# Kernel tuning notes

Hardware: AMD Instinct MI355X
Metric: run time of the kernel (lower is better)

The kernel has to match this reference:

```python
import jax, jax.numpy as jnp
import numpy as np

IN, H, OUT, T, B = 132, 1024, 132, 100, 256


def setup_inputs() -> dict:
    key = jax.random.key(0)
    ks = jax.random.split(key, 16)
    s_in = 1.0 / np.sqrt(H)
    def mk(k, shape):
        return jax.random.uniform(k, shape, jnp.float32, -s_in, s_in)
    inp = {
        "real_seq": jax.random.normal(ks[0], (B, T, IN), jnp.float32),
        "W_ih1": mk(ks[1], (4 * H, IN)), "W_hh1": mk(ks[2], (4 * H, H)),
        "b_ih1": mk(ks[3], (4 * H,)),   "b_hh1": mk(ks[4], (4 * H,)),
        "W_ih2": mk(ks[5], (4 * H, H)), "W_hh2": mk(ks[6], (4 * H, H)),
        "b_ih2": mk(ks[7], (4 * H,)),   "b_hh2": mk(ks[8], (4 * H,)),
        "W_ih3": mk(ks[9], (4 * H, H)), "W_hh3": mk(ks[10], (4 * H, H)),
        "b_ih3": mk(ks[11], (4 * H,)),  "b_hh3": mk(ks[12], (4 * H,)),
        "W_dec": mk(ks[13], (OUT, H)),  "b_dec": mk(ks[14], (OUT,)),
        "condition_num": 5, "groundtruth_num": 5,
    }
    return inp


def _lstm_cell(x, h, c, W_ih, W_hh, b_ih, b_hh):
    # torch LSTMCell: gates in (i, f, g, o) order
    gates = x @ W_ih.T + b_ih + h @ W_hh.T + b_hh
    i, f, g, o = jnp.split(gates, 4, axis=-1)
    i, f, o = jax.nn.sigmoid(i), jax.nn.sigmoid(f), jax.nn.sigmoid(o)
    g = jnp.tanh(g)
    c_new = f * c + i * g
    h_new = o * jnp.tanh(c_new)
    return h_new, c_new


def reference(real_seq, W_ih1, W_hh1, b_ih1, b_hh1,
              W_ih2, W_hh2, b_ih2, b_hh2,
              W_ih3, W_hh3, b_ih3, b_hh3,
              W_dec, b_dec, condition_num, groundtruth_num):
    batch, seq_len, _ = real_seq.shape
    # static teacher-forcing schedule: [1]*gt_num + [0]*cond_num, tiled
    gt = np.ones((100, groundtruth_num)); con = np.zeros((100, condition_num))
    cond = jnp.asarray(np.concatenate((gt, con), 1).reshape(-1)[:seq_len] == 1)

    z = jnp.zeros((batch, H), jnp.float32)
    init = (z, z, z, z, z, z, jnp.zeros((batch, OUT), jnp.float32))

    def step(carry, xs):
        h0, h1, h2, c0, c1, c2, prev_out = carry
        frame, use_gt = xs
        x = jnp.where(use_gt, frame, prev_out)
        # note: lstm2/lstm3 consume the OLD h0/h1, faithful to forward_lstm
        nh0, nc0 = _lstm_cell(x,  h0, c0, W_ih1, W_hh1, b_ih1, b_hh1)
        nh1, nc1 = _lstm_cell(h0, h1, c1, W_ih2, W_hh2, b_ih2, b_hh2)
        nh2, nc2 = _lstm_cell(h1, h2, c2, W_ih3, W_hh3, b_ih3, b_hh3)
        out = nh2 @ W_dec.T + b_dec
        return (nh0, nh1, nh2, nc0, nc1, nc2, out), out

    xs = (jnp.swapaxes(real_seq, 0, 1), cond)  # [T,B,IN], [T]
    _, outs = jax.lax.scan(step, init, xs)      # outs: [T,B,OUT]
    # torch concatenates along dim 1 each step -> [B, T*OUT]
    return jnp.swapaxes(outs, 0, 1).reshape(batch, seq_len * OUT)
```

## Files before the change

### kernel.cpp

```cpp
#include <hip/hip_runtime.h>
#include <math.h>

#define B_   256
#define T_   100
#define IN_  132
#define OUT_ 132
#define H_   1024
#define BH   ((size_t)B_ * H_)
#define WSZ  ((size_t)4096 * H_)

typedef _Float16 f16;
typedef _Float16 f16x8 __attribute__((ext_vector_type(8)));
typedef float    f32x4 __attribute__((ext_vector_type(4)));

#define MFMA16(a, b, c) __builtin_amdgcn_mfma_f32_16x16x32_f16((a), (b), (c), 0, 0, 0)

#define AS1 __attribute__((address_space(1)))
#define AS3 __attribute__((address_space(3)))

__device__ __forceinline__ void gl_lds16(const void* g, void* l) {
    __builtin_amdgcn_global_load_lds((AS1 void*)g, (AS3 void*)l, 16, 0, 0);
}

__device__ __forceinline__ float sigmoidf_(float x) {
    return 1.0f / (1.0f + __expf(-x));
}
__device__ __forceinline__ float tanhf_(float x) {
    float e = __expf(2.0f * x);
    return 1.0f - 2.0f / (e + 1.0f);
}


__global__ void conv_pad(const float* __restrict__ src, f16* __restrict__ dst,
                         int src_rows, int src_k, int dst_k) {
    int k = blockIdx.x * 256 + threadIdx.x;
    int r = blockIdx.y;
    if (k >= dst_k) return;
    float v = (r < src_rows && k < src_k) ? src[(size_t)r * src_k + k] : 0.0f;
    dst[(size_t)r * dst_k + k] = (f16)v;
}

__global__ void seq_pad(const float* __restrict__ src, f16* __restrict__ dst) {
    int k  = threadIdx.x;
    int bt = blockIdx.y;
    if (k >= 160) return;
    float v = (k < IN_) ? src[(size_t)bt * IN_ + k] : 0.0f;
    dst[(size_t)bt * 160 + k] = (f16)v;
}

__global__ void convT_kernel(const float* __restrict__ Wd, f16* __restrict__ WdT) {
    int k = blockIdx.x * 256 + threadIdx.x;
    int m = blockIdx.y;
    if (k >= 160) return;
    float v = (k < IN_) ? Wd[(size_t)k * H_ + m] : 0.0f;
    WdT[(size_t)m * 160 + k] = (f16)v;
}

__global__ void bias_add_kernel(const float* __restrict__ a, const float* __restrict__ b,
                                float* __restrict__ dst, int n) {
    int i = blockIdx.x * 256 + threadIdx.x;
    if (i < n) dst[i] = a[i] + b[i];
}

__global__ void bfb_kernel(const float* __restrict__ Wih1, const float* __restrict__ bd,
                           float* __restrict__ bfb) {
    int j = blockIdx.x * 256 + threadIdx.x;
    if (j >= 4096) return;
    float s = 0.0f;
    for (int k = 0; k < IN_; ++k) s += Wih1[(size_t)j * IN_ + k] * bd[k];
    bfb[j] = s;
}

__global__ void zero_kernel(float* __restrict__ p, int n) {
    int i = blockIdx.x * blockDim.x + threadIdx.x;
    int st = gridDim.x * blockDim.x;
    for (; i < n; i += st) p[i] = 0.0f;
}

__global__ __launch_bounds__(256) void wfb_mfma(
    const f16* __restrict__ W0, const f16* __restrict__ WdT, f16* __restrict__ Wfb)
{
    const int m0 = blockIdx.x * 128;
    const int n0 = blockIdx.y * 128;
    const int tid  = threadIdx.x;
    const int lane = tid & 63;
    const int w    = tid >> 6;
    const int lx   = lane & 15;
    const int quad = lane >> 4;
    const int wrow = w >> 1, wcol = w & 1;

    __shared__ __align__(16) char lds[32768];

    auto stA = [&](int kt, int buf) {
        char* base = lds + buf * 16384;
#pragma unroll
        for (int i = 0; i < 2; ++i) {
            int r  = w * 32 + i * 16 + (lane >> 2);
            int sg = (lane & 3) ^ (r & 3);
            const f16* g = W0 + (size_t)(m0 + r) * 160 + kt * 32 + sg * 8;
            gl_lds16(g, base + (size_t)(w * 32 + i * 16) * 64);
        }
    };
    auto stB = [&](int kt, int buf) {
        char* base = lds + 8192 + buf * 16384;
#pragma unroll
        for (int i = 0; i < 2; ++i) {
            int r  = w * 32 + i * 16 + (lane >> 2);
            int sg = (lane & 3) ^ (r & 3);
            const f16* g = WdT + (size_t)(n0 + r) * 160 + kt * 32 + sg * 8;
            gl_lds16(g, base + (size_t)(w * 32 + i * 16) * 64);
        }
    };

    f32x4 acc[4][4];
#pragma unroll
    for (int m = 0; m < 4; ++m)
#pragma unroll
        for (int n = 0; n < 4; ++n) acc[m][n] = (f32x4){0.f, 0.f, 0.f, 0.f};

    stA(0, 0); stB(0, 0);
    for (int kt = 0; kt < 5; ++kt) {
        __syncthreads();
        if (kt + 1 < 5) { stA(kt + 1, (kt + 1) & 1); stB(kt + 1, (kt + 1) & 1); }
        const char* bA = lds + (kt & 1) * 16384;
        const char* bB = lds + 8192 + (kt & 1) * 16384;
        f16x8 af[4], bf[4];
#pragma unroll
        for (int m = 0; m < 4; ++m) {
            int R = wrow * 64 + m * 16 + lx;
            af[m] = *(const f16x8*)(bA + R * 64 + ((quad ^ (R & 3)) * 16));
        }
#pragma unroll
        for (int n = 0; n < 4; ++n) {
            int R = wcol * 64 + n * 16 + lx;
            bf[n] = *(const f16x8*)(bB + R * 64 + ((quad ^ (R & 3)) * 16));
        }
#pragma unroll
        for (int m = 0; m < 4; ++m)
#pragma unroll
            for (int n = 0; n < 4; ++n)
                acc[m][n] = MFMA16(af[m], bf[n], acc[m][n]);
    }

#pragma unroll
    for (int m = 0; m < 4; ++m)
#pragma unroll
        for (int n = 0; n < 4; ++n)
#pragma unroll
            for (int r = 0; r < 4; ++r) {
                int row = m0 + wrow * 64 + m * 16 + quad * 4 + r;
                int col = n0 + wcol * 64 + n * 16 + lx;
                Wfb[(size_t)row * H_ + col] = (f16)acc[m][n][r];
            }
}

__global__ __launch_bounds__(256) void step_mfma(
    const f16* __restrict__ seq16,
    const f16* __restrict__ hfb,
    const f16* __restrict__ h2old,
    const f16* __restrict__ h01c,
    f16* __restrict__ h01n,
    f16* __restrict__ h2out,
    float* __restrict__ c_st,
    const f16* __restrict__ W0,
    const f16* __restrict__ Wb,
    const f16* __restrict__ Wfb,
    const float* __restrict__ bias_comb,
    const float* __restrict__ bfb,
    const int* __restrict__ cnum, const int* __restrict__ gnum,
    int t)
{
    const int j0   = blockIdx.x * 32;
    const int mb   = blockIdx.y;
    const int l    = blockIdx.z;
    const int tid  = threadIdx.x;
    const int lane = tid & 63;
    const int w    = tid >> 6;
    const int lx   = lane & 15;
    const int quad = lane >> 4;
    const int wrow = w >> 1, wcol = w & 1;

    __shared__ __align__(16) char lds[49152];

    bool use_gt = false;
    int n0 = 32;
    size_t ldA0 = H_, ldB0 = H_;
    const f16 *Ap0 = nullptr, *Wp0 = nullptr;
    if (l == 0) {
        int cn = cnum[0], gn = gnum[0];
        use_gt = (t % (cn + gn)) < gn;
        if (use_gt)      { Ap0 = seq16 + (size_t)t * 160; ldA0 = (size_t)T_ * 160;
                           Wp0 = W0; ldB0 = 160; n0 = 5; }
        else if (t == 0) { n0 = 0; }
        else             { Ap0 = hfb; Wp0 = Wfb; }
    } else if (l == 1) { Ap0 = h01c;      Wp0 = Wb + 1 * WSZ; }
    else               { Ap0 = h01c + BH; Wp0 = Wb + 3 * WSZ; }
    const f16* Ap1 = (l == 0) ? h01c : (l == 1) ? (h01c + BH) : h2old;
    const f16* Wp1 = Wb + (size_t)((l == 0) ? 0 : (l == 1) ? 2 : 4) * WSZ;
    const int ntot = n0 + 32;

    auto stA = [&](const f16* Ap, size_t ldA, int kk, int buf) {
        char* base = lds + buf * 12288 + w * 1024;
        int row = w * 16 + (lane >> 2);
        int sg  = (lane & 3) ^ (row & 3);
        const f16* g = Ap + (size_t)(mb * 64 + row) * ldA + kk * 32 + sg * 8;
        gl_lds16(g, base);
    };
    auto stB = [&](const f16* Wp, size_t ldk, int kk, int buf) {
        char* base = lds + buf * 12288 + 4096;
#pragma unroll
        for (int i = 0; i < 2; ++i) {
            int c    = w * 32 + i * 16 + (lane >> 2);
            int sg   = (lane & 3) ^ (c & 3);
            int gate = (c >> 4) & 3;
            int jj   = (c & 15) + (c >> 6) * 16;
            const f16* g = Wp + (size_t)(gate * H_ + j0 + jj) * ldk + kk * 32 + sg * 8;
            gl_lds16(g, base + (size_t)(w * 32 + i * 16) * 64);
        }
    };
    auto stage = [&](int kt, int buf) {
        if (kt < n0) {
            stA(Ap0, ldA0, kt, buf);
            stB(Wp0, ldB0, kt, buf);
        } else {
            stA(Ap1, (size_t)H_, kt - n0, buf);
            stB(Wp1, (size_t)H_, kt - n0, buf);
        }
    };

    f32x4 acc[2][4];
#pragma unroll
    for (int m = 0; m < 2; ++m)
#pragma unroll
        for (int n = 0; n < 4; ++n) acc[m][n] = (f32x4){0.f, 0.f, 0.f, 0.f};

    stage(0, 0);
    stage(1, 1);
    stage(2, 2);

    for (int kt = 0; kt < ntot; ++kt) {
        if (kt < ntot - 2)       asm volatile("s_waitcnt vmcnt(6)" ::: "memory");
        else if (kt == ntot - 2) asm volatile("s_waitcnt vmcnt(3)" ::: "memory");
        else                     asm volatile("s_waitcnt vmcnt(0)" ::: "memory");
        __builtin_amdgcn_s_barrier();

        const char* bA = lds + (kt & 3) * 12288;
        const char* bB = bA + 4096;
        f16x8 af[2], bf[4];
#pragma unroll
        for (int m = 0; m < 2; ++m) {
            int R = wrow * 32 + m * 16 + lx;
            af[m] = *(const f16x8*)(bA + R * 64 + ((quad ^ (R & 3)) * 16));
        }
#pragma unroll
        for (int n = 0; n < 4; ++n) {
            int R = wcol * 64 + n * 16 + lx;
            bf[n] = *(const f16x8*)(bB + R * 64 + ((quad ^ (R & 3)) * 16));
        }
        asm volatile("s_waitcnt lgkmcnt(0)" ::: "memory");
        __builtin_amdgcn_sched_barrier(0);
        __builtin_amdgcn_s_barrier();

        if (kt + 3 < ntot) stage(kt + 3, (kt + 3) & 3);

        __builtin_amdgcn_s_setprio(1);
#pragma unroll
        for (int m = 0; m < 2; ++m)
#pragma unroll
            for (int n = 0; n < 4; ++n)
                acc[m][n] = MFMA16(af[m], bf[n], acc[m][n]);
        __builtin_amdgcn_s_setprio(0);
    }

    const int j = j0 + wcol * 16 + lx;
    const float* bc = bias_comb + l * 4096;
    const bool addfb = (l == 0 && !use_gt && t > 0);
    float bi  = bc[j]        + (addfb ? bfb[j]        : 0.f);
    float bff = bc[1024 + j] + (addfb ? bfb[1024 + j] : 0.f);
    float bg  = bc[2048 + j] + (addfb ? bfb[2048 + j] : 0.f);
    float bo  = bc[3072 + j] + (addfb ? bfb[3072 + j] : 0.f);
#pragma unroll
    for (int m = 0; m < 2; ++m) {
#pragma unroll
        for (int r = 0; r < 4; ++r) {
            int b = mb * 64 + wrow * 32 + m * 16 + quad * 4 + r;
            float gi = acc[m][0][r] + bi;
            float gf = acc[m][1][r] + bff;
            float gg = acc[m][2][r] + bg;
            float go = acc[m][3][r] + bo;
            size_t ix = ((size_t)l * B_ + b) * H_ + j;
            float cn = sigmoidf_(gf) * c_st[ix] + sigmoidf_(gi) * tanhf_(gg);
            c_st[ix] = cn;
            float hv = sigmoidf_(go) * tanhf_(cn);
            if (l == 2) h2out[(size_t)b * H_ + j] = (f16)hv;
            else        h01n[(size_t)l * BH + (size_t)b * H_ + j] = (f16)hv;
        }
    }
}

__global__ __launch_bounds__(256) void decode_mfma(
    const f16* __restrict__ hist,
    const f16* __restrict__ Wd16,
    const float* __restrict__ bd,
    float* __restrict__ dout)
{
    const int r0  = blockIdx.x * 128;
    const int nb0 = blockIdx.y * 32;
    const int tid  = threadIdx.x;
    const int lane = tid & 63;
    const int w    = tid >> 6;
    const int lx   = lane & 15;
    const int quad = lane >> 4;

    __shared__ __align__(16) char lds[20480];

    auto stA = [&](int kt, int buf) {
        char* base = lds + buf * 10240;
#pragma unroll
        for (int i = 0; i < 2; ++i) {
            int r  = w * 32 + i * 16 + (lane >> 2);
            int sg = (lane & 3) ^ (r & 3);
            const f16* g = hist + (size_t)(r0 + r) * H_ + kt * 32 + sg * 8;
            gl_lds16(g, base + (size_t)(w * 32 + i * 16) * 64);
        }
    };
    auto stB = [&](int kt, int buf) {
        char* base = lds + 8192 + buf * 10240;
        if (w < 2) {
            int r  = w * 16 + (lane >> 2);
            int sg = (lane & 3) ^ (r & 3);
            const f16* g = Wd16 + (size_t)(nb0 + r) * H_ + kt * 32 + sg * 8;
            gl_lds16(g, base + (size_t)(w * 16) * 64);
        }
    };

    f32x4 acc[2][2];
#pragma unroll
    for (int m = 0; m < 2; ++m)
#pragma unroll
        for (int n = 0; n < 2; ++n) acc[m][n] = (f32x4){0.f, 0.f, 0.f, 0.f};

    stA(0, 0); stB(0, 0);
    for (int kt = 0; kt < 32; ++kt) {
        __syncthreads();
        if (kt + 1 < 32) { stA(kt + 1, (kt + 1) & 1); stB(kt + 1, (kt + 1) & 1); }
        const char* bA = lds + (kt & 1) * 10240;
        const char* bB = lds + 8192 + (kt & 1) * 10240;
        f16x8 af[2], bf[2];
#pragma unroll
        for (int m = 0; m < 2; ++m) {
            int R = w * 32 + m * 16 + lx;
            af[m] = *(const f16x8*)(bA + R * 64 + ((quad ^ (R & 3)) * 16));
        }
#pragma unroll
        for (int n = 0; n < 2; ++n) {
            int R = n * 16 + lx;
            bf[n] = *(const f16x8*)(bB + R * 64 + ((quad ^ (R & 3)) * 16));
        }
#pragma unroll
        for (int m = 0; m < 2; ++m)
#pragma unroll
            for (int n = 0; n < 2; ++n)
                acc[m][n] = MFMA16(af[m], bf[n], acc[m][n]);
    }

#pragma unroll
    for (int n = 0; n < 2; ++n) {
        int nn = nb0 + n * 16 + lx;
        if (nn < OUT_) {
            float bv = bd[nn];
#pragma unroll
            for (int m = 0; m < 2; ++m)
#pragma unroll
                for (int r = 0; r < 4; ++r) {
                    int row = r0 + w * 32 + m * 16 + quad * 4 + r;
                    int tt = row >> 8, b = row & 255;
                    dout[(size_t)b * (T_ * OUT_) + (size_t)tt * OUT_ + nn] = acc[m][n][r] + bv;
                }
        }
    }
}


extern "C" void kernel_launch(void* const* d_in, const int* in_sizes, int n_in,
                              void* d_out, int out_size, void* d_ws, size_t ws_size,
                              hipStream_t stream) {
    const float* seq  = (const float*)d_in[0];
    const float* Wih1 = (const float*)d_in[1];
    const float* Whh1 = (const float*)d_in[2];
    const float* bih1 = (const float*)d_in[3];
    const float* bhh1 = (const float*)d_in[4];
    const float* Wih2 = (const float*)d_in[5];
    const float* Whh2 = (const float*)d_in[6];
    const float* bih2 = (const float*)d_in[7];
    const float* bhh2 = (const float*)d_in[8];
    const float* Wih3 = (const float*)d_in[9];
    const float* Whh3 = (const float*)d_in[10];
    const float* bih3 = (const float*)d_in[11];
    const float* bhh3 = (const float*)d_in[12];
    const float* Wd   = (const float*)d_in[13];
    const float* bd   = (const float*)d_in[14];
    const int*   cnum = (const int*)d_in[15];
    const int*   gnum = (const int*)d_in[16];

    char* p = (char*)d_ws;
    f16*  W0   = (f16*)p;  p += (size_t)4096 * 160 * 2;
    f16*  Wb   = (f16*)p;  p += (size_t)5 * 4096 * 1024 * 2;
    f16*  Wd16 = (f16*)p;  p += (size_t)160 * 1024 * 2;
    f16*  WdT  = (f16*)p;  p += (size_t)1024 * 160 * 2;
    f16*  Wfb  = (f16*)p;  p += (size_t)4096 * 1024 * 2;
    float* bias_comb = (float*)p; p += (size_t)3 * 4096 * 4;
    float* bfb = (float*)p; p += (size_t)4096 * 4;
    f16*  hist = (f16*)p;  p += (size_t)100 * BH * 2;
    f16*  h01a = (f16*)p;  p += (size_t)2 * BH * 2;
    f16*  h01b = (f16*)p;  p += (size_t)2 * BH * 2;
    float* c_st = (float*)p; p += (size_t)3 * BH * 4;
    f16*  seq16 = (f16*)p; p += (size_t)B_ * T_ * 160 * 2;
    const int zero_floats = (int)(((size_t)4 * BH * 2 + (size_t)3 * BH * 4) / 4);

    conv_pad<<<dim3(1, 4096), 256, 0, stream>>>(Wih1, W0, 4096, IN_, 160);
    conv_pad<<<dim3(4, 4096), 256, 0, stream>>>(Whh1, Wb + 0 * WSZ, 4096, H_, H_);
    conv_pad<<<dim3(4, 4096), 256, 0, stream>>>(Wih2, Wb + 1 * WSZ, 4096, H_, H_);
    conv_pad<<<dim3(4, 4096), 256, 0, stream>>>(Whh2, Wb + 2 * WSZ, 4096, H_, H_);
    conv_pad<<<dim3(4, 4096), 256, 0, stream>>>(Wih3, Wb + 3 * WSZ, 4096, H_, H_);
    conv_pad<<<dim3(4, 4096), 256, 0, stream>>>(Whh3, Wb + 4 * WSZ, 4096, H_, H_);
    conv_pad<<<dim3(4, 160), 256, 0, stream>>>(Wd, Wd16, OUT_, H_, H_);
    convT_kernel<<<dim3(1, 1024), 256, 0, stream>>>(Wd, WdT);
    seq_pad<<<dim3(1, B_ * T_), 256, 0, stream>>>(seq, seq16);
    bias_add_kernel<<<16, 256, 0, stream>>>(bih1, bhh1, bias_comb + 0 * 4096, 4096);
    bias_add_kernel<<<16, 256, 0, stream>>>(bih2, bhh2, bias_comb + 1 * 4096, 4096);
    bias_add_kernel<<<16, 256, 0, stream>>>(bih3, bhh3, bias_comb + 2 * 4096, 4096);
    bfb_kernel<<<16, 256, 0, stream>>>(Wih1, bd, bfb);
    wfb_mfma<<<dim3(32, 8), 256, 0, stream>>>(W0, WdT, Wfb);
    zero_kernel<<<512, 256, 0, stream>>>((float*)h01a, zero_floats);

    f16 *hc = h01a, *hn = h01b;
    for (int t = 0; t < T_; ++t) {
        const f16* hfb   = (t > 0) ? (hist + (size_t)(t - 1) * BH) : hc;
        const f16* h2old = (t > 0) ? (hist + (size_t)(t - 1) * BH) : hc;
        step_mfma<<<dim3(32, 4, 3), 256, 0, stream>>>(
            seq16, hfb, h2old, hc, hn, hist + (size_t)t * BH, c_st,
            W0, Wb, Wfb, bias_comb, bfb, cnum, gnum, t);
        f16* tmp = hc; hc = hn; hn = tmp;
    }

    decode_mfma<<<dim3(200, 5), 256, 0, stream>>>(hist, Wd16, bd, (float*)d_out);
}
```

Measured before the change: 3.151 ms.

## Split LSTM step K-loop across two warp teams with full-batch tiles

The step kernel now uses 512-thread blocks covering all 256 batch rows and 16 hidden units per gate, so each weight tile is loaded once per step instead of once per batch block. Two 4-wave teams split the reduction: one handles the input/feedback matrix and the other the recurrent matrix, and the partial sums are combined through LDS before the gate epilogue. The grid shrinks from 384 to 192 blocks and each block uses 160KB of dynamic LDS, which limits each CU to one block. The aim is less redundant weight traffic and a shorter serial K loop, at the cost of parallelism, idle time in team 0 when its K range is short, and an extra LDS reduction.

```diff
diff --git a/kernel.cpp b/kernel.cpp
--- a/kernel.cpp
+++ b/kernel.cpp
@@ -154,7 +154,7 @@
             }
 }
 
-__global__ __launch_bounds__(256) void step_mfma(
+__global__ __launch_bounds__(512) void step_mfma(
     const f16* __restrict__ seq16,
     const f16* __restrict__ hfb,
     const f16* __restrict__ h2old,
@@ -170,130 +170,145 @@
     const int* __restrict__ cnum, const int* __restrict__ gnum,
     int t)
 {
-    const int j0   = blockIdx.x * 32;
-    const int mb   = blockIdx.y;
-    const int l    = blockIdx.z;
+    extern __shared__ __align__(16) char lds[];
+
+    const int j0   = blockIdx.x * 16;
+    const int l    = blockIdx.y;
     const int tid  = threadIdx.x;
     const int lane = tid & 63;
     const int w    = tid >> 6;
+    const int team = w >> 2;
+    const int w4   = w & 3;
     const int lx   = lane & 15;
     const int quad = lane >> 4;
-    const int wrow = w >> 1, wcol = w & 1;
-
-    __shared__ __align__(16) char lds[49152];
 
     bool use_gt = false;
-    int n0 = 32;
-    size_t ldA0 = H_, ldB0 = H_;
-    const f16 *Ap0 = nullptr, *Wp0 = nullptr;
-    if (l == 0) {
-        int cn = cnum[0], gn = gnum[0];
-        use_gt = (t % (cn + gn)) < gn;
-        if (use_gt)      { Ap0 = seq16 + (size_t)t * 160; ldA0 = (size_t)T_ * 160;
-                           Wp0 = W0; ldB0 = 160; n0 = 5; }
-        else if (t == 0) { n0 = 0; }
-        else             { Ap0 = hfb; Wp0 = Wfb; }
-    } else if (l == 1) { Ap0 = h01c;      Wp0 = Wb + 1 * WSZ; }
-    else               { Ap0 = h01c + BH; Wp0 = Wb + 3 * WSZ; }
-    const f16* Ap1 = (l == 0) ? h01c : (l == 1) ? (h01c + BH) : h2old;
-    const f16* Wp1 = Wb + (size_t)((l == 0) ? 0 : (l == 1) ? 2 : 4) * WSZ;
-    const int ntot = n0 + 32;
-
-    auto stA = [&](const f16* Ap, size_t ldA, int kk, int buf) {
-        char* base = lds + buf * 12288 + w * 1024;
-        int row = w * 16 + (lane >> 2);
-        int sg  = (lane & 3) ^ (row & 3);
-        const f16* g = Ap + (size_t)(mb * 64 + row) * ldA + kk * 32 + sg * 8;
-        gl_lds16(g, base);
+    int nt = 32;
+    size_t ldA = H_, ldk = H_;
+    const f16 *Ap = h01c, *Wp = Wb;
+    if (team == 0) {
+        if (l == 0) {
+            int cn = cnum[0], gn = gnum[0];
+            use_gt = (t % (cn + gn)) < gn;
+            if (use_gt)      { Ap = seq16 + (size_t)t * 160; ldA = (size_t)T_ * 160;
+                               Wp = W0; ldk = 160; nt = 5; }
+            else if (t == 0) { nt = 0; }
+            else             { Ap = hfb; Wp = Wfb; }
+        } else if (l == 1) { Ap = h01c;      Wp = Wb + 1 * WSZ; }
+        else               { Ap = h01c + BH; Wp = Wb + 3 * WSZ; }
+    } else {
+        Ap = (l == 0) ? h01c : (l == 1) ? (h01c + BH) : h2old;
+        Wp = Wb + (size_t)((l == 0) ? 0 : (l == 1) ? 2 : 4) * WSZ;
+    }
+
+    char* tb = lds + team * 81920;
+    auto stage = [&](int kt, int buf) {
+        char* base = tb + buf * 20480;
+#pragma unroll
+        for (int i = 0; i < 4; ++i) {
+            int row = w4 * 64 + i * 16 + (lane >> 2);
+            int sg  = (lane & 3) ^ (row & 3);
+            gl_lds16(Ap + (size_t)row * ldA + kt * 32 + sg * 8,
+                     base + (size_t)(w4 * 64 + i * 16) * 64);
+        }
+        {
+            int c  = w4 * 16 + (lane >> 2);
+            int sg = (lane & 3) ^ (c & 3);
+            gl_lds16(Wp + (size_t)(w4 * H_ + j0 + (c & 15)) * ldk + kt * 32 + sg * 8,
+                     base + 16384 + (size_t)w4 * 1024);
+        }
     };
-    auto stB = [&](const f16* Wp, size_t ldk, int kk, int buf) {
-        char* base = lds + buf * 12288 + 4096;
-#pragma unroll
-        for (int i = 0; i < 2; ++i) {
-            int c    = w * 32 + i * 16 + (lane >> 2);
-            int sg   = (lane & 3) ^ (c & 3);
-            int gate = (c >> 4) & 3;
-            int jj   = (c & 15) + (c >> 6) * 16;
-            const f16* g = Wp + (size_t)(gate * H_ + j0 + jj) * ldk + kk * 32 + sg * 8;
-            gl_lds16(g, base + (size_t)(w * 32 + i * 16) * 64);
-        }
-    };
-    auto stage = [&](int kt, int buf) {
-        if (kt < n0) {
-            stA(Ap0, ldA0, kt, buf);
-            stB(Wp0, ldB0, kt, buf);
-        } else {
-            stA(Ap1, (size_t)H_, kt - n0, buf);
-            stB(Wp1, (size_t)H_, kt - n0, buf);
-        }
-    };
-
-    f32x4 acc[2][4];
-#pragma unroll
-    for (int m = 0; m < 2; ++m)
+
+    f32x4 acc[4][4];
+#pragma unroll
+    for (int m = 0; m < 4; ++m)
 #pragma unroll
         for (int n = 0; n < 4; ++n) acc[m][n] = (f32x4){0.f, 0.f, 0.f, 0.f};
 
-    stage(0, 0);
-    stage(1, 1);
-    stage(2, 2);
-
-    for (int kt = 0; kt < ntot; ++kt) {
-        if (kt < ntot - 2)       asm volatile("s_waitcnt vmcnt(6)" ::: "memory");
-        else if (kt == ntot - 2) asm volatile("s_waitcnt vmcnt(3)" ::: "memory");
-        else                     asm volatile("s_waitcnt vmcnt(0)" ::: "memory");
+    if (0 < nt) stage(0, 0);
+    if (1 < nt) stage(1, 1);
+    if (2 < nt) stage(2, 2);
+
+    for (int kt = 0; kt < 32; ++kt) {
+        const bool act = kt < nt;
+        if (act) {
+            if (kt < nt - 2)       asm volatile("s_waitcnt vmcnt(10)" ::: "memory");
+            else if (kt == nt - 2) asm volatile("s_waitcnt vmcnt(5)" ::: "memory");
+            else                   asm volatile("s_waitcnt vmcnt(0)" ::: "memory");
+        }
         __builtin_amdgcn_s_barrier();
 
-        const char* bA = lds + (kt & 3) * 12288;
-        const char* bB = bA + 4096;
-        f16x8 af[2], bf[4];
-#pragma unroll
-        for (int m = 0; m < 2; ++m) {
-            int R = wrow * 32 + m * 16 + lx;
-            af[m] = *(const f16x8*)(bA + R * 64 + ((quad ^ (R & 3)) * 16));
-        }
-#pragma unroll
-        for (int n = 0; n < 4; ++n) {
-            int R = wcol * 64 + n * 16 + lx;
-            bf[n] = *(const f16x8*)(bB + R * 64 + ((quad ^ (R & 3)) * 16));
+        f16x8 af[4], bf[4];
+        if (act) {
+            const char* bA = tb + (kt & 3) * 20480;
+            const char* bB = bA + 16384;
+#pragma unroll
+            for (int m = 0; m < 4; ++m) {
+                int R = w4 * 64 + m * 16 + lx;
+                af[m] = *(const f16x8*)(bA + R * 64 + ((quad ^ (R & 3)) * 16));
+            }
+#pragma unroll
+            for (int n = 0; n < 4; ++n) {
+                int R = n * 16 + lx;
+                bf[n] = *(const f16x8*)(bB + R * 64 + ((quad ^ (R & 3)) * 16));
+            }
         }
         asm volatile("s_waitcnt lgkmcnt(0)" ::: "memory");
         __builtin_amdgcn_sched_barrier(0);
         __builtin_amdgcn_s_barrier();
 
-        if (kt + 3 < ntot) stage(kt + 3, (kt + 3) & 3);
-
-        __builtin_amdgcn_s_setprio(1);
-#pragma unroll
-        for (int m = 0; m < 2; ++m)
+        if (kt + 3 < nt) stage(kt + 3, (kt + 3) & 3);
+
+        if (act) {
+            __builtin_amdgcn_s_setprio(1);
+#pragma unroll
+            for (int m = 0; m < 4; ++m)
+#pragma unroll
+                for (int n = 0; n < 4; ++n)
+                    acc[m][n] = MFMA16(af[m], bf[n], acc[m][n]);
+            __builtin_amdgcn_s_setprio(0);
+        }
+    }
+
+    __syncthreads();
+    float* exch = (float*)(lds + 81920);
+    if (team == 1) {
+#pragma unroll
+        for (int m = 0; m < 4; ++m)
 #pragma unroll
             for (int n = 0; n < 4; ++n)
-                acc[m][n] = MFMA16(af[m], bf[n], acc[m][n]);
-        __builtin_amdgcn_s_setprio(0);
-    }
-
-    const int j = j0 + wcol * 16 + lx;
-    const float* bc = bias_comb + l * 4096;
-    const bool addfb = (l == 0 && !use_gt && t > 0);
-    float bi  = bc[j]        + (addfb ? bfb[j]        : 0.f);
-    float bff = bc[1024 + j] + (addfb ? bfb[1024 + j] : 0.f);
-    float bg  = bc[2048 + j] + (addfb ? bfb[2048 + j] : 0.f);
-    float bo  = bc[3072 + j] + (addfb ? bfb[3072 + j] : 0.f);
-#pragma unroll
-    for (int m = 0; m < 2; ++m) {
-#pragma unroll
-        for (int r = 0; r < 4; ++r) {
-            int b = mb * 64 + wrow * 32 + m * 16 + quad * 4 + r;
-            float gi = acc[m][0][r] + bi;
-            float gf = acc[m][1][r] + bff;
-            float gg = acc[m][2][r] + bg;
-            float go = acc[m][3][r] + bo;
-            size_t ix = ((size_t)l * B_ + b) * H_ + j;
-            float cn = sigmoidf_(gf) * c_st[ix] + sigmoidf_(gi) * tanhf_(gg);
-            c_st[ix] = cn;
-            float hv = sigmoidf_(go) * tanhf_(cn);
-            if (l == 2) h2out[(size_t)b * H_ + j] = (f16)hv;
-            else        h01n[(size_t)l * BH + (size_t)b * H_ + j] = (f16)hv;
+#pragma unroll
+                for (int r = 0; r < 4; ++r) {
+                    int row = w4 * 64 + m * 16 + quad * 4 + r;
+                    exch[row * 68 + n * 16 + lx] = acc[m][n][r];
+                }
+    }
+    __syncthreads();
+
+    if (team == 0) {
+        const int j = j0 + lx;
+        const float* bc = bias_comb + l * 4096;
+        const bool addfb = (l == 0 && !use_gt && t > 0);
+        float bi  = bc[j]        + (addfb ? bfb[j]        : 0.f);
+        float bff = bc[1024 + j] + (addfb ? bfb[1024 + j] : 0.f);
+        float bg  = bc[2048 + j] + (addfb ? bfb[2048 + j] : 0.f);
+        float bo  = bc[3072 + j] + (addfb ? bfb[3072 + j] : 0.f);
+#pragma unroll
+        for (int m = 0; m < 4; ++m) {
+#pragma unroll
+            for (int r = 0; r < 4; ++r) {
+                int b = w4 * 64 + m * 16 + quad * 4 + r;
+                float gi = acc[m][0][r] + exch[b * 68 + lx]      + bi;
+                float gf = acc[m][1][r] + exch[b * 68 + 16 + lx] + bff;
+                float gg = acc[m][2][r] + exch[b * 68 + 32 + lx] + bg;
+                float go = acc[m][3][r] + exch[b * 68 + 48 + lx] + bo;
+                size_t ix = ((size_t)l * B_ + b) * H_ + j;
+                float cn2 = sigmoidf_(gf) * c_st[ix] + sigmoidf_(gi) * tanhf_(gg);
+                c_st[ix] = cn2;
+                float hv = sigmoidf_(go) * tanhf_(cn2);
+                if (l == 2) h2out[(size_t)b * H_ + j] = (f16)hv;
+                else        h01n[(size_t)l * BH + (size_t)b * H_ + j] = (f16)hv;
+            }
         }
     }
 }
@@ -418,6 +433,9 @@
     f16*  seq16 = (f16*)p; p += (size_t)B_ * T_ * 160 * 2;
     const int zero_floats = (int)(((size_t)4 * BH * 2 + (size_t)3 * BH * 4) / 4);
 
+    hipFuncSetAttribute((const void*)step_mfma,
+                        hipFuncAttributeMaxDynamicSharedMemorySize, 163840);
+
     conv_pad<<<dim3(1, 4096), 256, 0, stream>>>(Wih1, W0, 4096, IN_, 160);
     conv_pad<<<dim3(4, 4096), 256, 0, stream>>>(Whh1, Wb + 0 * WSZ, 4096, H_, H_);
     conv_pad<<<dim3(4, 4096), 256, 0, stream>>>(Wih2, Wb + 1 * WSZ, 4096, H_, H_);
@@ -438,7 +456,7 @@
     for (int t = 0; t < T_; ++t) {
         const f16* hfb   = (t > 0) ? (hist + (size_t)(t - 1) * BH) : hc;
         const f16* h2old = (t > 0) ? (hist + (size_t)(t - 1) * BH) : hc;
-        step_mfma<<<dim3(32, 4, 3), 256, 0, stream>>>(
+        step_mfma<<<dim3(64, 3), 512, 163840, stream>>>(
             seq16, hfb, h2old, hc, hn, hist + (size_t)t * BH, c_st,
             W0, Wb, Wfb, bias_comb, bfb, cnum, gnum, t);
         f16* tmp = hc; hc = hn; hn = tmp;
```

Result: slower. 3.724 ms (+18.2%).

## Pre-pack weights, inputs and hidden states into tile-contiguous layout for LDS staging

Applied to the files above, without the earlier changes.

Adds packing kernels that rearrange the recurrent weights, input projection, feedback weights and the input sequence into 32x32-tile contiguous blocks matching the step kernel's LDS tile layout. Hidden states are now written in the same packed layout (with a separate unpacked copy of h2 kept for decoding), so each global-to-LDS load in the step kernel reads a contiguous 4KB/1KB chunk instead of strided rows. The intent is more coalesced global loads and simpler address arithmetic in the hot per-timestep GEMM. The cost is extra one-time packing kernels, more workspace, and an extra store of h2 per step.

```diff
diff --git a/kernel.cpp b/kernel.cpp
--- a/kernel.cpp
+++ b/kernel.cpp
@@ -7,7 +7,6 @@
 #define OUT_ 132
 #define H_   1024
 #define BH   ((size_t)B_ * H_)
-#define WSZ  ((size_t)4096 * H_)
 
 typedef _Float16 f16;
 typedef _Float16 f16x8 __attribute__((ext_vector_type(8)));
@@ -40,14 +39,6 @@
     dst[(size_t)r * dst_k + k] = (f16)v;
 }
 
-__global__ void seq_pad(const float* __restrict__ src, f16* __restrict__ dst) {
-    int k  = threadIdx.x;
-    int bt = blockIdx.y;
-    if (k >= 160) return;
-    float v = (k < IN_) ? src[(size_t)bt * IN_ + k] : 0.0f;
-    dst[(size_t)bt * 160 + k] = (f16)v;
-}
-
 __global__ void convT_kernel(const float* __restrict__ Wd, f16* __restrict__ WdT) {
     int k = blockIdx.x * 256 + threadIdx.x;
     int m = blockIdx.y;
@@ -75,6 +66,69 @@
     int i = blockIdx.x * blockDim.x + threadIdx.x;
     int st = gridDim.x * blockDim.x;
     for (; i < n; i += st) p[i] = 0.0f;
+}
+
+__global__ __launch_bounds__(256) void pack_w(const float* __restrict__ W,
+                                              f16* __restrict__ Wpk, int wsel) {
+    int jt = blockIdx.x, kt = blockIdx.y;
+    f16* dst = Wpk + (((size_t)wsel * 32 + jt) * 32 + kt) * 4096;
+    for (int u = threadIdx.x; u < 512; u += 256) {
+        int c = u >> 2, ch = u & 3;
+        int gate = (c >> 4) & 3, jj = (c & 15) + (c >> 6) * 16;
+        const float* s = W + ((size_t)gate * 1024 + jt * 32 + jj) * 1024 + kt * 32 + ch * 8;
+        f16x8 v;
+#pragma unroll
+        for (int e = 0; e < 8; ++e) v[e] = (f16)s[e];
+        *(f16x8*)(dst + (size_t)u * 8) = v;
+    }
+}
+
+__global__ __launch_bounds__(256) void pack_wf16(const f16* __restrict__ W,
+                                                 f16* __restrict__ Wpk, int wsel) {
+    int jt = blockIdx.x, kt = blockIdx.y;
+    f16* dst = Wpk + (((size_t)wsel * 32 + jt) * 32 + kt) * 4096;
+    for (int u = threadIdx.x; u < 512; u += 256) {
+        int c = u >> 2, ch = u & 3;
+        int gate = (c >> 4) & 3, jj = (c & 15) + (c >> 6) * 16;
+        const f16* s = W + ((size_t)gate * 1024 + jt * 32 + jj) * 1024 + kt * 32 + ch * 8;
+        f16x8 v = *(const f16x8*)s;
+        *(f16x8*)(dst + (size_t)u * 8) = v;
+    }
+}
+
+__global__ __launch_bounds__(256) void pack_w0(const float* __restrict__ W,
+                                               f16* __restrict__ W0pk) {
+    int jt = blockIdx.x, kt = blockIdx.y;
+    f16* dst = W0pk + ((size_t)jt * 5 + kt) * 4096;
+    for (int u = threadIdx.x; u < 512; u += 256) {
+        int c = u >> 2, ch = u & 3;
+        int gate = (c >> 4) & 3, jj = (c & 15) + (c >> 6) * 16;
+        int row = gate * 1024 + jt * 32 + jj;
+        f16x8 v;
+#pragma unroll
+        for (int e = 0; e < 8; ++e) {
+            int k = kt * 32 + ch * 8 + e;
+            v[e] = (f16)((k < IN_) ? W[(size_t)row * IN_ + k] : 0.0f);
+        }
+        *(f16x8*)(dst + (size_t)u * 8) = v;
+    }
+}
+
+__global__ __launch_bounds__(256) void pack_seq(const float* __restrict__ seq,
+                                                f16* __restrict__ seqpk) {
+    int kt = blockIdx.x, t = blockIdx.y;
+    int b = threadIdx.x;
+    f16* d = seqpk + (((size_t)t * 5 + kt) * 256 + b) * 32;
+#pragma unroll
+    for (int ch = 0; ch < 4; ++ch) {
+        f16x8 v;
+#pragma unroll
+        for (int e = 0; e < 8; ++e) {
+            int k = kt * 32 + ch * 8 + e;
+            v[e] = (f16)((k < IN_) ? seq[((size_t)b * T_ + t) * IN_ + k] : 0.0f);
+        }
+        *(f16x8*)(d + ch * 8) = v;
+    }
 }
 
 __global__ __launch_bounds__(256) void wfb_mfma(
@@ -155,22 +209,21 @@
 }
 
 __global__ __launch_bounds__(256) void step_mfma(
-    const f16* __restrict__ seq16,
-    const f16* __restrict__ hfb,
-    const f16* __restrict__ h2old,
-    const f16* __restrict__ h01c,
-    f16* __restrict__ h01n,
-    f16* __restrict__ h2out,
+    const f16* __restrict__ seqpk,
+    const f16* __restrict__ h2pkP,
+    const f16* __restrict__ h01pkC,
+    f16* __restrict__ h01pkN,
+    f16* __restrict__ h2pkN,
+    f16* __restrict__ histN,
     float* __restrict__ c_st,
-    const f16* __restrict__ W0,
-    const f16* __restrict__ Wb,
-    const f16* __restrict__ Wfb,
+    const f16* __restrict__ W0pk,
+    const f16* __restrict__ Wpk,
     const float* __restrict__ bias_comb,
     const float* __restrict__ bfb,
     const int* __restrict__ cnum, const int* __restrict__ gnum,
     int t)
 {
-    const int j0   = blockIdx.x * 32;
+    const int jt   = blockIdx.x;
     const int mb   = blockIdx.y;
     const int l    = blockIdx.z;
     const int tid  = threadIdx.x;
@@ -184,48 +237,36 @@
 
     bool use_gt = false;
     int n0 = 32;
-    size_t ldA0 = H_, ldB0 = H_;
-    const f16 *Ap0 = nullptr, *Wp0 = nullptr;
+    const char *A0 = nullptr, *B0 = nullptr;
+    const char* wb = (const char*)Wpk + (size_t)jt * 262144;
     if (l == 0) {
         int cn = cnum[0], gn = gnum[0];
         use_gt = (t % (cn + gn)) < gn;
-        if (use_gt)      { Ap0 = seq16 + (size_t)t * 160; ldA0 = (size_t)T_ * 160;
-                           Wp0 = W0; ldB0 = 160; n0 = 5; }
+        if (use_gt)      { A0 = (const char*)(seqpk + (size_t)t * 5 * 8192);
+                           B0 = (const char*)(W0pk + (size_t)jt * 5 * 4096); n0 = 5; }
         else if (t == 0) { n0 = 0; }
-        else             { Ap0 = hfb; Wp0 = Wfb; }
-    } else if (l == 1) { Ap0 = h01c;      Wp0 = Wb + 1 * WSZ; }
-    else               { Ap0 = h01c + BH; Wp0 = Wb + 3 * WSZ; }
-    const f16* Ap1 = (l == 0) ? h01c : (l == 1) ? (h01c + BH) : h2old;
-    const f16* Wp1 = Wb + (size_t)((l == 0) ? 0 : (l == 1) ? 2 : 4) * WSZ;
+        else             { A0 = (const char*)h2pkP; B0 = wb + (size_t)5 * 8388608; }
+    } else if (l == 1) { A0 = (const char*)h01pkC;        B0 = wb + (size_t)1 * 8388608; }
+    else               { A0 = (const char*)(h01pkC + BH); B0 = wb + (size_t)3 * 8388608; }
+    const char* A1 = (l == 0) ? (const char*)h01pkC
+                   : (l == 1) ? (const char*)(h01pkC + BH) : (const char*)h2pkP;
+    const char* B1 = wb + (size_t)((l == 0) ? 0 : (l == 1) ? 2 : 4) * 8388608;
     const int ntot = n0 + 32;
 
-    auto stA = [&](const f16* Ap, size_t ldA, int kk, int buf) {
-        char* base = lds + buf * 12288 + w * 1024;
-        int row = w * 16 + (lane >> 2);
-        int sg  = (lane & 3) ^ (row & 3);
-        const f16* g = Ap + (size_t)(mb * 64 + row) * ldA + kk * 32 + sg * 8;
-        gl_lds16(g, base);
-    };
-    auto stB = [&](const f16* Wp, size_t ldk, int kk, int buf) {
-        char* base = lds + buf * 12288 + 4096;
-#pragma unroll
-        for (int i = 0; i < 2; ++i) {
-            int c    = w * 32 + i * 16 + (lane >> 2);
-            int sg   = (lane & 3) ^ (c & 3);
-            int gate = (c >> 4) & 3;
-            int jj   = (c & 15) + (c >> 6) * 16;
-            const f16* g = Wp + (size_t)(gate * H_ + j0 + jj) * ldk + kk * 32 + sg * 8;
-            gl_lds16(g, base + (size_t)(w * 32 + i * 16) * 64);
-        }
-    };
+    const int lr = lane >> 2, lc = lane & 3;
+    const int perl = lr * 64 + ((lc ^ (lr & 3)) * 16);
+
     auto stage = [&](int kt, int buf) {
-        if (kt < n0) {
-            stA(Ap0, ldA0, kt, buf);
-            stB(Wp0, ldB0, kt, buf);
-        } else {
-            stA(Ap1, (size_t)H_, kt - n0, buf);
-            stB(Wp1, (size_t)H_, kt - n0, buf);
-        }
+        const char *pA, *pB; int kk;
+        if (kt < n0) { kk = kt;      pA = A0; pB = B0; }
+        else         { kk = kt - n0; pA = A1; pB = B1; }
+        char* base = lds + buf * 12288;
+        gl_lds16(pA + (size_t)kk * 16384 + (size_t)(mb * 64 + w * 16) * 64 + perl,
+                 base + w * 1024);
+#pragma unroll
+        for (int i = 0; i < 2; ++i)
+            gl_lds16(pB + (size_t)kk * 8192 + (size_t)(w * 2 + i) * 1024 + perl,
+                     base + 4096 + (size_t)(w * 2 + i) * 1024);
     };
 
     f32x4 acc[2][4];
@@ -272,7 +313,7 @@
         __builtin_amdgcn_s_setprio(0);
     }
 
-    const int j = j0 + wcol * 16 + lx;
+    const int j = jt * 32 + wcol * 16 + lx;
     const float* bc = bias_comb + l * 4096;
     const bool addfb = (l == 0 && !use_gt && t > 0);
     float bi  = bc[j]        + (addfb ? bfb[j]        : 0.f);
@@ -292,8 +333,10 @@
             float cn = sigmoidf_(gf) * c_st[ix] + sigmoidf_(gi) * tanhf_(gg);
             c_st[ix] = cn;
             float hv = sigmoidf_(go) * tanhf_(cn);
-            if (l == 2) h2out[(size_t)b * H_ + j] = (f16)hv;
-            else        h01n[(size_t)l * BH + (size_t)b * H_ + j] = (f16)hv;
+            f16 hv16 = (f16)hv;
+            size_t pix = ((size_t)(j >> 5) * 256 + b) * 32 + (j & 31);
+            if (l == 2) { h2pkN[pix] = hv16; histN[(size_t)b * H_ + j] = hv16; }
+            else        h01pkN[(size_t)l * BH + pix] = hv16;
         }
     }
 }
@@ -405,43 +448,49 @@
 
     char* p = (char*)d_ws;
     f16*  W0   = (f16*)p;  p += (size_t)4096 * 160 * 2;
-    f16*  Wb   = (f16*)p;  p += (size_t)5 * 4096 * 1024 * 2;
     f16*  Wd16 = (f16*)p;  p += (size_t)160 * 1024 * 2;
     f16*  WdT  = (f16*)p;  p += (size_t)1024 * 160 * 2;
     f16*  Wfb  = (f16*)p;  p += (size_t)4096 * 1024 * 2;
     float* bias_comb = (float*)p; p += (size_t)3 * 4096 * 4;
     float* bfb = (float*)p; p += (size_t)4096 * 4;
     f16*  hist = (f16*)p;  p += (size_t)100 * BH * 2;
-    f16*  h01a = (f16*)p;  p += (size_t)2 * BH * 2;
-    f16*  h01b = (f16*)p;  p += (size_t)2 * BH * 2;
-    float* c_st = (float*)p; p += (size_t)3 * BH * 4;
-    f16*  seq16 = (f16*)p; p += (size_t)B_ * T_ * 160 * 2;
-    const int zero_floats = (int)(((size_t)4 * BH * 2 + (size_t)3 * BH * 4) / 4);
+    f16*  h01pkA = (f16*)p; p += (size_t)2 * BH * 2;
+    f16*  h2pkA  = (f16*)p; p += (size_t)BH * 2;
+    float* c_st  = (float*)p; p += (size_t)3 * BH * 4;
+    f16*  h01pkB = (f16*)p; p += (size_t)2 * BH * 2;
+    f16*  h2pkB  = (f16*)p; p += (size_t)BH * 2;
+    f16*  Wpk   = (f16*)p; p += (size_t)6 * 32 * 32 * 4096 * 2;
+    f16*  W0pk  = (f16*)p; p += (size_t)32 * 5 * 4096 * 2;
+    f16*  seqpk = (f16*)p; p += (size_t)T_ * 5 * 256 * 32 * 2;
+
+    const int zero_floats = (int)(((size_t)3 * BH * 2 + (size_t)3 * BH * 4) / 4);
 
     conv_pad<<<dim3(1, 4096), 256, 0, stream>>>(Wih1, W0, 4096, IN_, 160);
-    conv_pad<<<dim3(4, 4096), 256, 0, stream>>>(Whh1, Wb + 0 * WSZ, 4096, H_, H_);
-    conv_pad<<<dim3(4, 4096), 256, 0, stream>>>(Wih2, Wb + 1 * WSZ, 4096, H_, H_);
-    conv_pad<<<dim3(4, 4096), 256, 0, stream>>>(Whh2, Wb + 2 * WSZ, 4096, H_, H_);
-    conv_pad<<<dim3(4, 4096), 256, 0, stream>>>(Wih3, Wb + 3 * WSZ, 4096, H_, H_);
-    conv_pad<<<dim3(4, 4096), 256, 0, stream>>>(Whh3, Wb + 4 * WSZ, 4096, H_, H_);
     conv_pad<<<dim3(4, 160), 256, 0, stream>>>(Wd, Wd16, OUT_, H_, H_);
     convT_kernel<<<dim3(1, 1024), 256, 0, stream>>>(Wd, WdT);
-    seq_pad<<<dim3(1, B_ * T_), 256, 0, stream>>>(seq, seq16);
     bias_add_kernel<<<16, 256, 0, stream>>>(bih1, bhh1, bias_comb + 0 * 4096, 4096);
     bias_add_kernel<<<16, 256, 0, stream>>>(bih2, bhh2, bias_comb + 1 * 4096, 4096);
     bias_add_kernel<<<16, 256, 0, stream>>>(bih3, bhh3, bias_comb + 2 * 4096, 4096);
     bfb_kernel<<<16, 256, 0, stream>>>(Wih1, bd, bfb);
     wfb_mfma<<<dim3(32, 8), 256, 0, stream>>>(W0, WdT, Wfb);
-    zero_kernel<<<512, 256, 0, stream>>>((float*)h01a, zero_floats);
-
-    f16 *hc = h01a, *hn = h01b;
+    pack_w<<<dim3(32, 32), 256, 0, stream>>>(Whh1, Wpk, 0);
+    pack_w<<<dim3(32, 32), 256, 0, stream>>>(Wih2, Wpk, 1);
+    pack_w<<<dim3(32, 32), 256, 0, stream>>>(Whh2, Wpk, 2);
+    pack_w<<<dim3(32, 32), 256, 0, stream>>>(Wih3, Wpk, 3);
+    pack_w<<<dim3(32, 32), 256, 0, stream>>>(Whh3, Wpk, 4);
+    pack_wf16<<<dim3(32, 32), 256, 0, stream>>>(Wfb, Wpk, 5);
+    pack_w0<<<dim3(32, 5), 256, 0, stream>>>(Wih1, W0pk);
+    pack_seq<<<dim3(5, T_), 256, 0, stream>>>(seq, seqpk);
+    zero_kernel<<<512, 256, 0, stream>>>((float*)h01pkA, zero_floats);
+
+    f16 *h01C = h01pkA, *h01N = h01pkB, *h2P = h2pkA, *h2N = h2pkB;
     for (int t = 0; t < T_; ++t) {
-        const f16* hfb   = (t > 0) ? (hist + (size_t)(t - 1) * BH) : hc;
-        const f16* h2old = (t > 0) ? (hist + (size_t)(t - 1) * BH) : hc;
         step_mfma<<<dim3(32, 4, 3), 256, 0, stream>>>(
-            seq16, hfb, h2old, hc, hn, hist + (size_t)t * BH, c_st,
-            W0, Wb, Wfb, bias_comb, bfb, cnum, gnum, t);
-        f16* tmp = hc; hc = hn; hn = tmp;
+            seqpk, h2P, h01C, h01N, h2N, hist + (size_t)t * BH, c_st,
+            W0pk, Wpk, bias_comb, bfb, cnum, gnum, t);
+        f16* tmp;
+        tmp = h01C; h01C = h01N; h01N = tmp;
+        tmp = h2P;  h2P  = h2N;  h2N  = tmp;
     }
 
     decode_mfma<<<dim3(200, 5), 256, 0, stream>>>(hist, Wd16, bd, (float*)d_out);
```

Result: faster. 3.020 ms (-4.2%).
